# Kernel tuning notes

Hardware: AMD Instinct MI355X
Metric: run time of the kernel (lower is better)

Reference implementation:

```python
import jax, jax.numpy as jnp
import numpy as np

EPS = 1e-5
GROUPS = 8

def setup_inputs() -> dict:
    key = jax.random.key(0)
    ks = jax.random.split(key, 7)
    b, c, h, w = 32, 256, 32, 32
    x = jax.random.normal(ks[0], (b, c, h, w), dtype=jnp.float32)
    gn_w = jax.random.normal(ks[1], (c,), dtype=jnp.float32) * 0.02 + 1.0
    gn_b = jax.random.normal(ks[2], (c,), dtype=jnp.float32) * 0.02
    qkv_w = jax.random.normal(ks[3], (3 * c, c), dtype=jnp.float32) / np.sqrt(c)
    qkv_b = jax.random.normal(ks[4], (3 * c,), dtype=jnp.float32) * 0.02
    out_w = jax.random.normal(ks[5], (c, c), dtype=jnp.float32) / np.sqrt(c)
    out_b = jax.random.normal(ks[6], (c,), dtype=jnp.float32) * 0.02
    return {"x": x, "gn_w": gn_w, "gn_b": gn_b, "qkv_w": qkv_w,
            "qkv_b": qkv_b, "out_w": out_w, "out_b": out_b}

def _group_norm(x, w, b):
    B, C, H, W = x.shape
    xg = x.reshape(B, GROUPS, C // GROUPS, H, W)
    mu = jnp.mean(xg, axis=(2, 3, 4), keepdims=True)
    var = jnp.var(xg, axis=(2, 3, 4), keepdims=True)
    xn = ((xg - mu) * jax.lax.rsqrt(var + EPS)).reshape(B, C, H, W)
    return xn * w[None, :, None, None] + b[None, :, None, None]

def reference(x, gn_w, gn_b, qkv_w, qkv_b, out_w, out_b):
    b, c, h, w = x.shape
    n = h * w
    xn = _group_norm(x, gn_w, gn_b)                       # [b,c,h,w]
    # 1x1 conv == channel matmul
    qkv = jnp.einsum('bchw,oc->bohw', xn, qkv_w) + qkv_b[None, :, None, None]
    q, k, v = jnp.split(qkv, 3, axis=1)                   # each [b,c,h,w]
    q = q.reshape(b, c, n).transpose(0, 2, 1)             # [b,n,c]
    k = k.reshape(b, c, n).transpose(0, 2, 1)
    v = v.reshape(b, c, n).transpose(0, 2, 1)
    scores = jnp.einsum('bnc,bmc->bnm', q, k) / jnp.sqrt(jnp.float32(c))
    attn = jax.nn.softmax(scores, axis=-1)                # [b,n,n]
    out = jnp.einsum('bnm,bmc->bnc', attn, v)             # [b,n,c]
    out = out.transpose(0, 2, 1).reshape(b, c, h, w)
    out = jnp.einsum('bchw,oc->bohw', out, out_w) + out_b[None, :, None, None]
    # NOTE: torch code reassigns x = group_norm(x), so residual is the normalized x
    return out + xn
```

## Files before the change

kernel.cpp:

```cpp
#include <hip/hip_runtime.h>
#include <hip/hip_bf16.h>

typedef __bf16 bf16;
typedef __bf16 bf16x4 __attribute__((ext_vector_type(4)));
typedef __bf16 bf16x8 __attribute__((ext_vector_type(8)));
typedef float f32x4 __attribute__((ext_vector_type(4)));

#define B_  32
#define C_  256
#define N_  1024
#define G_  8
#define CG_ 32
#define O3_ 768

#define SWZ9(el) ((el) ^ ((((el) >> 8) & 15) << 3))
#define SWZ7(el) ((el) ^ ((((el) >> 6) & 7) << 3))

#define GLOAD16(gp, lp)                                                        \
    __builtin_amdgcn_global_load_lds(                                          \
        (const __attribute__((address_space(1))) void*)(gp),                   \
        (__attribute__((address_space(3))) void*)(lp), 16, 0, 0)

__global__ __launch_bounds__(256) void k_gnconv(const float* __restrict__ x,
                                                const float* __restrict__ w,
                                                const float* __restrict__ bia,
                                                bf16* __restrict__ xn,
                                                bf16* __restrict__ xt,
                                                const float* __restrict__ qkv_w,
                                                const float* __restrict__ out_w,
                                                bf16* __restrict__ qkv_wh,
                                                bf16* __restrict__ out_wh) {
    int blk = blockIdx.x;
    int tid = threadIdx.x;
    if (blk >= 256) {
        int i = (blk - 256) * 256 + tid;
        if (i < O3_ * C_) qkv_wh[i] = (bf16)qkv_w[i];
        if (i < C_ * C_)  out_wh[i] = (bf16)out_w[i];
        return;
    }

    extern __shared__ char smem[];
    float* xs   = (float*)smem;
    float4* xs4 = (float4*)smem;
    bf16* tile  = (bf16*)(smem + 131072);
    int b = blk >> 3, g = blk & 7;
    const float4* xb4 = (const float4*)(x + (size_t)b * C_ * N_ + (size_t)g * CG_ * N_);

    float s = 0.f, ss = 0.f;
    for (int i = tid; i < CG_ * N_ / 4; i += 256) {
        float4 v = xb4[i];
        xs4[i] = v;
        s  += v.x + v.y + v.z + v.w;
        ss += v.x * v.x + v.y * v.y + v.z * v.z + v.w * v.w;
    }
    for (int off = 32; off; off >>= 1) {
        s  += __shfl_down(s, off);
        ss += __shfl_down(ss, off);
    }
    __shared__ float red[8];
    __shared__ float stat[2];
    int wid = tid >> 6, lane = tid & 63;
    if (lane == 0) { red[wid] = s; red[wid + 4] = ss; }
    __syncthreads();
    if (tid == 0) {
        float S  = red[0] + red[1] + red[2] + red[3];
        float SS = red[4] + red[5] + red[6] + red[7];
        float mu = S / (float)(CG_ * N_);
        float var = SS / (float)(CG_ * N_) - mu * mu;
        stat[0] = mu;
        stat[1] = rsqrtf(var + 1e-5f);
    }
    __syncthreads();
    float mu = stat[0], rstd = stat[1];

    for (int nc = 0; nc < N_; nc += 256) {
        for (int i = tid; i < 2048; i += 256) {
            int cl = i >> 6, f = i & 63;
            int c = g * CG_ + cl;
            float sc = rstd * w[c], sh = bia[c] - mu * sc;
            float4 v = xs4[cl * 256 + (nc >> 2) + f];
            bf16x4 h = { (bf16)(v.x * sc + sh), (bf16)(v.y * sc + sh),
                         (bf16)(v.z * sc + sh), (bf16)(v.w * sc + sh) };
            *(bf16x4*)(xn + (size_t)b * C_ * N_ + (size_t)c * N_ + nc + f * 4) = h;
            tile[(f * 4 + 0) * 40 + cl] = h[0];
            tile[(f * 4 + 1) * 40 + cl] = h[1];
            tile[(f * 4 + 2) * 40 + cl] = h[2];
            tile[(f * 4 + 3) * 40 + cl] = h[3];
        }
        __syncthreads();
        for (int u = tid; u < 256 * 4; u += 256) {
            int nl = u >> 2, ch = u & 3;
            bf16x8 v = *(const bf16x8*)&tile[nl * 40 + ch * 8];
            *(bf16x8*)(xt + (size_t)b * N_ * C_ + (size_t)(nc + nl) * C_ + g * CG_ + ch * 8) = v;
        }
        __syncthreads();
    }
}

__global__ __launch_bounds__(256) void k_qkv(const bf16* __restrict__ xt,
                                             const bf16* __restrict__ wq,
                                             const float* __restrict__ qb,
                                             bf16* __restrict__ Qs,
                                             bf16* __restrict__ Kt,
                                             bf16* __restrict__ Vt) {
    __shared__ bf16 smem[17408];
    bf16* aT = smem;
    bf16* bT = smem + 8192;
    int nt = blockIdx.x, ot = blockIdx.y, b = blockIdx.z;
    int tid = threadIdx.x, wid = tid >> 6, lane = tid & 63;
    int wr = wid >> 1, wc = wid & 1;
    const bf16* Ab = xt + (size_t)b * N_ * C_ + (size_t)nt * 128 * C_;
    const bf16* Bb = wq + (size_t)ot * 128 * C_;

    bf16x8 areg[4], breg[4];
    #define LOAD_KT(kt)                                                        \
        for (int j = 0; j < 4; ++j) {                                          \
            int lin = (j * 256 + tid) * 8;                                     \
            int row = lin >> 6, col = lin & 63;                                \
            areg[j] = *(const bf16x8*)&Ab[(size_t)row * C_ + (kt) * 64 + col]; \
            breg[j] = *(const bf16x8*)&Bb[(size_t)row * C_ + (kt) * 64 + col]; \
        }

    f32x4 acc[4][4] = {};
    LOAD_KT(0);
    for (int kt = 0; kt < 4; ++kt) {
        for (int j = 0; j < 4; ++j) {
            int lin = (j * 256 + tid) * 8;
            *(bf16x8*)&aT[SWZ7(lin)] = areg[j];
            *(bf16x8*)&bT[SWZ7(lin)] = breg[j];
        }
        __syncthreads();
        if (kt < 3) { LOAD_KT(kt + 1); }
        for (int kk = 0; kk < 2; ++kk) {
            bf16x8 af[4], bfr[4];
            for (int m = 0; m < 4; ++m) {
                int el = (wr * 64 + m * 16 + (lane & 15)) * 64 + kk * 32 + (lane >> 4) * 8;
                af[m] = *(const bf16x8*)&aT[SWZ7(el)];
            }
            for (int n = 0; n < 4; ++n) {
                int el = (wc * 64 + n * 16 + (lane & 15)) * 64 + kk * 32 + (lane >> 4) * 8;
                bfr[n] = *(const bf16x8*)&bT[SWZ7(el)];
            }
            for (int m = 0; m < 4; ++m)
                for (int n = 0; n < 4; ++n)
                    acc[m][n] = __builtin_amdgcn_mfma_f32_16x16x32_bf16(af[m], bfr[n], acc[m][n], 0, 0, 0);
        }
        __syncthreads();
    }
    #undef LOAD_KT

    int o0 = ot * 128;
    if (ot < 4) {
        bf16* dst = (ot < 2) ? (Qs + (size_t)b * N_ * C_) : (Kt + (size_t)b * N_ * C_);
        float qsc = (ot < 2) ? 0.0625f : 1.0f;
        for (int m = 0; m < 4; ++m) for (int n = 0; n < 4; ++n) {
            int o = o0 + wc * 64 + n * 16 + (lane & 15);
            float bias = qb[o];
            int row0 = nt * 128 + wr * 64 + m * 16 + (lane >> 4) * 4;
            for (int r = 0; r < 4; ++r)
                dst[(size_t)(row0 + r) * C_ + (o & 255)] = (bf16)((acc[m][n][r] + bias) * qsc);
        }
    } else {
        bf16* tileE = smem;
        for (int m = 0; m < 4; ++m) for (int n = 0; n < 4; ++n) {
            int ol = wc * 64 + n * 16 + (lane & 15);
            float bias = qb[o0 + ol];
            int rl0 = wr * 64 + m * 16 + (lane >> 4) * 4;
            for (int r = 0; r < 4; ++r)
                tileE[(size_t)ol * 136 + rl0 + r] = (bf16)(acc[m][n][r] + bias);
        }
        __syncthreads();
        bf16* Vb = Vt + (size_t)b * C_ * N_ + (size_t)(o0 - 512) * N_ + (size_t)nt * 128;
        for (int u = tid; u < 128 * 16; u += 256) {
            int ol = u >> 4, ch = u & 15;
            bf16x8 v = *(const bf16x8*)&tileE[ol * 136 + ch * 8];
            *(bf16x8*)&Vb[(size_t)ol * N_ + ch * 8] = v;
        }
    }
}

__global__ __launch_bounds__(256, 2) void k_attn(const bf16* __restrict__ Qs,
                                                 const bf16* __restrict__ Kt,
                                                 const bf16* __restrict__ Vt,
                                                 bf16* __restrict__ Ao) {
    extern __shared__ char smem[];
    bf16*  kbuf = (bf16*)smem;
    bf16*  vbuf = (bf16*)(smem + 32768);
    bf16*  pl   = (bf16*)(smem + 65536);
    float* al   = (float*)(smem + 70656);
    int b = blockIdx.x, qb = blockIdx.y;
    int tid = threadIdx.x, wid = tid >> 6, lane = tid & 63;
    const bf16* Qb = Qs + (size_t)b * N_ * C_;
    const bf16* Kb = Kt + (size_t)b * N_ * C_;
    const bf16* Vb = Vt + (size_t)b * C_ * N_;
    int q0 = qb * 64;

    bf16x8 qf[8];
    {
        int row = q0 + wid * 16 + (lane & 15);
        const bf16* qr = Qb + (size_t)row * C_ + (lane >> 4) * 8;
        #pragma unroll
        for (int kk = 0; kk < 8; ++kk) qf[kk] = *(const bf16x8*)(qr + kk * 32);
    }

    f32x4 oac[4][4] = {};
    float lrun[4] = {0.f, 0.f, 0.f, 0.f};

    auto stage = [&](int mt, int bi) {
        int m0 = mt * 32;
        bf16* kd = kbuf + bi * 8192;
        bf16* vd = vbuf + bi * 8192;
        #pragma unroll
        for (int j = 0; j < 4; ++j) {
            int chunk = wid * 4 + j;
            int d = chunk * 512 + lane * 8;
            int ek = SWZ9(d);
            int krow = ek >> 8, kcol = ek & 255;
            GLOAD16(Kb + (size_t)(m0 + krow) * C_ + kcol, kd + chunk * 512);
            int ev = SWZ7(d);
            int kv = ev & 31;
            int ch = ((ev >> 6) << 1) | ((ev >> 5) & 1);
            GLOAD16(Vb + (size_t)ch * N_ + m0 + kv, vd + chunk * 512);
        }
    };

    stage(0, 0);
    __syncthreads();

    for (int mt = 0; mt < 32; ++mt) {
        int cur = mt & 1;
        if (mt < 31) stage(mt + 1, cur ^ 1);

        const bf16* kc = kbuf + cur * 8192;
        const bf16* vc = vbuf + cur * 8192;

        f32x4 sac[2] = {};
        __builtin_amdgcn_s_setprio(1);
        #pragma unroll
        for (int kk = 0; kk < 8; ++kk)
            #pragma unroll
            for (int n = 0; n < 2; ++n) {
                int el = (n * 16 + (lane & 15)) * 256 + kk * 32 + (lane >> 4) * 8;
                bf16x8 bfr = *(const bf16x8*)&kc[SWZ9(el)];
                sac[n] = __builtin_amdgcn_mfma_f32_16x16x32_bf16(qf[kk], bfr, sac[n], 0, 0, 0);
            }
        __builtin_amdgcn_s_setprio(0);

        #pragma unroll
        for (int r = 0; r < 4; ++r) {
            int prow = (wid * 16 + (lane >> 4) * 4 + r) * 40 + (lane & 15);
            float e0 = __expf(fminf(sac[0][r], 60.f));
            float e1 = __expf(fminf(sac[1][r], 60.f));
            lrun[r] += e0 + e1;
            pl[prow]      = (bf16)e0;
            pl[prow + 16] = (bf16)e1;
        }
        __syncthreads();

        __builtin_amdgcn_s_setprio(1);
        bf16x8 paf[4];
        #pragma unroll
        for (int m = 0; m < 4; ++m)
            paf[m] = *(const bf16x8*)&pl[(m * 16 + (lane & 15)) * 40 + (lane >> 4) * 8];
        #pragma unroll
        for (int n = 0; n < 4; ++n) {
            int ch = wid * 64 + n * 16 + (lane & 15);
            int e = (ch >> 1) * 64 + (ch & 1) * 32 + (lane >> 4) * 8;
            bf16x8 bfr = *(const bf16x8*)&vc[SWZ7(e)];
            #pragma unroll
            for (int m = 0; m < 4; ++m)
                oac[m][n] = __builtin_amdgcn_mfma_f32_16x16x32_bf16(paf[m], bfr, oac[m][n], 0, 0, 0);
        }
        __builtin_amdgcn_s_setprio(0);

        __syncthreads();
    }

    #pragma unroll
    for (int r = 0; r < 4; ++r) {
        float s = lrun[r];
        s += __shfl_xor(s, 1);
        s += __shfl_xor(s, 2);
        s += __shfl_xor(s, 4);
        s += __shfl_xor(s, 8);
        lrun[r] = s;
    }
    if (!(lane & 15)) {
        #pragma unroll
        for (int r = 0; r < 4; ++r)
            al[wid * 16 + (lane >> 4) * 4 + r] = 1.f / lrun[r];
    }
    __syncthreads();

    #pragma unroll
    for (int m = 0; m < 4; ++m)
        #pragma unroll
        for (int r = 0; r < 4; ++r) {
            float iv = al[m * 16 + (lane >> 4) * 4 + r];
            int row = q0 + m * 16 + (lane >> 4) * 4 + r;
            #pragma unroll
            for (int n = 0; n < 4; ++n)
                Ao[(size_t)b * N_ * C_ + (size_t)row * C_ + wid * 64 + n * 16 + (lane & 15)] =
                    (bf16)(oac[m][n][r] * iv);
        }
}

__global__ __launch_bounds__(256) void k_proj(const bf16* __restrict__ Ao,
                                              const bf16* __restrict__ wo,
                                              const float* __restrict__ ob,
                                              const bf16* __restrict__ xn,
                                              float* __restrict__ out) {
    __shared__ bf16 aT[128 * 64];
    __shared__ bf16 bT[128 * 64];
    int nt = blockIdx.x, ot = blockIdx.y, b = blockIdx.z;
    int tid = threadIdx.x, wid = tid >> 6, lane = tid & 63;
    int wr = wid >> 1, wc = wid & 1;
    const bf16* Abase = wo + (size_t)ot * 128 * C_;
    const bf16* Bbase = Ao + (size_t)b * N_ * C_ + (size_t)nt * 128 * C_;

    bf16x8 areg[4], breg[4];
    #define LOAD_KT(kt)                                                            \
        for (int j = 0; j < 4; ++j) {                                              \
            int lin = (j * 256 + tid) * 8;                                         \
            int row = lin >> 6, col = lin & 63;                                    \
            areg[j] = *(const bf16x8*)&Abase[(size_t)row * C_ + (kt) * 64 + col];  \
            breg[j] = *(const bf16x8*)&Bbase[(size_t)row * C_ + (kt) * 64 + col];  \
        }

    f32x4 acc[4][4] = {};
    LOAD_KT(0);
    for (int kt = 0; kt < 4; ++kt) {
        for (int j = 0; j < 4; ++j) {
            int lin = (j * 256 + tid) * 8;
            *(bf16x8*)&aT[SWZ7(lin)] = areg[j];
            *(bf16x8*)&bT[SWZ7(lin)] = breg[j];
        }
        __syncthreads();
        if (kt < 3) { LOAD_KT(kt + 1); }
        for (int kk = 0; kk < 2; ++kk) {
            bf16x8 af[4], bfr[4];
            for (int m = 0; m < 4; ++m) {
                int el = (wr * 64 + m * 16 + (lane & 15)) * 64 + kk * 32 + (lane >> 4) * 8;
                af[m] = *(const bf16x8*)&aT[SWZ7(el)];
            }
            for (int n = 0; n < 4; ++n) {
                int el = (wc * 64 + n * 16 + (lane & 15)) * 64 + kk * 32 + (lane >> 4) * 8;
                bfr[n] = *(const bf16x8*)&bT[SWZ7(el)];
            }
            for (int m = 0; m < 4; ++m)
                for (int n = 0; n < 4; ++n)
                    acc[m][n] = __builtin_amdgcn_mfma_f32_16x16x32_bf16(af[m], bfr[n], acc[m][n], 0, 0, 0);
        }
        __syncthreads();
    }
    #undef LOAD_KT

    for (int m = 0; m < 4; ++m) {
        int o0 = ot * 128 + wr * 64 + m * 16 + (lane >> 4) * 4;
        for (int n = 0; n < 4; ++n) {
            int col = nt * 128 + wc * 64 + n * 16 + (lane & 15);
            for (int r = 0; r < 4; ++r) {
                int o = o0 + r;
                float v = acc[m][n][r] + ob[o] + (float)xn[(size_t)b * C_ * N_ + (size_t)o * N_ + col];
                out[(size_t)b * C_ * N_ + (size_t)o * N_ + col] = v;
            }
        }
    }
}

extern "C" void kernel_launch(void* const* d_in, const int* in_sizes, int n_in,
                              void* d_out, int out_size, void* d_ws, size_t ws_size,
                              hipStream_t stream) {
    const float* x     = (const float*)d_in[0];
    const float* gn_w  = (const float*)d_in[1];
    const float* gn_b  = (const float*)d_in[2];
    const float* qkv_w = (const float*)d_in[3];
    const float* qkv_b = (const float*)d_in[4];
    const float* out_w = (const float*)d_in[5];
    const float* out_b = (const float*)d_in[6];
    float* out = (float*)d_out;

    char* ws = (char*)d_ws;
    size_t tensor = (size_t)B_ * C_ * N_ * 2;
    bf16* xn  = (bf16*)(ws);
    bf16* xt  = (bf16*)(ws + tensor);
    bf16* Qs  = (bf16*)(ws + 2 * tensor);
    bf16* Kt  = (bf16*)(ws + 3 * tensor);
    bf16* Vt  = (bf16*)(ws + 4 * tensor);
    bf16* Ao  = xt;
    bf16* qkv_wh = (bf16*)(ws + 5 * tensor);
    bf16* out_wh = (bf16*)(ws + 5 * tensor + (size_t)O3_ * C_ * 2);

    (void)hipFuncSetAttribute(reinterpret_cast<const void*>(&k_gnconv),
                              hipFuncAttributeMaxDynamicSharedMemorySize, 151552);
    (void)hipFuncSetAttribute(reinterpret_cast<const void*>(&k_attn),
                              hipFuncAttributeMaxDynamicSharedMemorySize, 70912);

    k_gnconv<<<1024, 256, 151552, stream>>>(x, gn_w, gn_b, xn, xt,
                                            qkv_w, out_w, qkv_wh, out_wh);
    k_qkv<<<dim3(8, 6, 32), 256, 0, stream>>>(xt, qkv_wh, qkv_b, Qs, Kt, Vt);
    k_attn<<<dim3(32, 16), 256, 70912, stream>>>(Qs, Kt, Vt, Ao);
    k_proj<<<dim3(8, 2, 32), 256, 0, stream>>>(Ao, out_wh, out_b, xn, out);
}
```

Before: 117.4 us.

## Fuse output projection and residual into attention kernel epilogue

The separate projection kernel is removed. Each attention block now writes its normalized 64x256 output tile into shared memory and multiplies it by the out-projection weights with MFMA, reading the weights straight from global memory. It then adds the bias and the normalized-input residual before storing. This saves one kernel launch and the global round-trip of the attention output. In exchange the attention kernel carries an extra GEMM epilogue with uncached weight loads and column-strided output stores.

New measurement: 112.3 us. 1.05x faster.

```diff
diff --git a/kernel.cpp b/kernel.cpp
--- a/kernel.cpp
+++ b/kernel.cpp
@@ -40,7 +40,6 @@
     }
 
     extern __shared__ char smem[];
-    float* xs   = (float*)smem;
     float4* xs4 = (float4*)smem;
     bf16* tile  = (bf16*)(smem + 131072);
     int b = blk >> 3, g = blk & 7;
@@ -182,12 +181,16 @@
 __global__ __launch_bounds__(256, 2) void k_attn(const bf16* __restrict__ Qs,
                                                  const bf16* __restrict__ Kt,
                                                  const bf16* __restrict__ Vt,
-                                                 bf16* __restrict__ Ao) {
+                                                 const bf16* __restrict__ wo,
+                                                 const float* __restrict__ ob,
+                                                 const bf16* __restrict__ xn,
+                                                 float* __restrict__ out) {
     extern __shared__ char smem[];
     bf16*  kbuf = (bf16*)smem;
     bf16*  vbuf = (bf16*)(smem + 32768);
     bf16*  pl   = (bf16*)(smem + 65536);
     float* al   = (float*)(smem + 70656);
+    bf16*  Osm  = (bf16*)smem;
     int b = blockIdx.x, qb = blockIdx.y;
     int tid = threadIdx.x, wid = tid >> 6, lane = tid & 63;
     const bf16* Qb = Qs + (size_t)b * N_ * C_;
@@ -297,72 +300,45 @@
         #pragma unroll
         for (int r = 0; r < 4; ++r) {
             float iv = al[m * 16 + (lane >> 4) * 4 + r];
-            int row = q0 + m * 16 + (lane >> 4) * 4 + r;
+            int row = m * 16 + (lane >> 4) * 4 + r;
             #pragma unroll
             for (int n = 0; n < 4; ++n)
-                Ao[(size_t)b * N_ * C_ + (size_t)row * C_ + wid * 64 + n * 16 + (lane & 15)] =
-                    (bf16)(oac[m][n][r] * iv);
-        }
-}
-
-__global__ __launch_bounds__(256) void k_proj(const bf16* __restrict__ Ao,
-                                              const bf16* __restrict__ wo,
-                                              const float* __restrict__ ob,
-                                              const bf16* __restrict__ xn,
-                                              float* __restrict__ out) {
-    __shared__ bf16 aT[128 * 64];
-    __shared__ bf16 bT[128 * 64];
-    int nt = blockIdx.x, ot = blockIdx.y, b = blockIdx.z;
-    int tid = threadIdx.x, wid = tid >> 6, lane = tid & 63;
-    int wr = wid >> 1, wc = wid & 1;
-    const bf16* Abase = wo + (size_t)ot * 128 * C_;
-    const bf16* Bbase = Ao + (size_t)b * N_ * C_ + (size_t)nt * 128 * C_;
-
-    bf16x8 areg[4], breg[4];
-    #define LOAD_KT(kt)                                                            \
-        for (int j = 0; j < 4; ++j) {                                              \
-            int lin = (j * 256 + tid) * 8;                                         \
-            int row = lin >> 6, col = lin & 63;                                    \
-            areg[j] = *(const bf16x8*)&Abase[(size_t)row * C_ + (kt) * 64 + col];  \
-            breg[j] = *(const bf16x8*)&Bbase[(size_t)row * C_ + (kt) * 64 + col];  \
-        }
-
-    f32x4 acc[4][4] = {};
-    LOAD_KT(0);
-    for (int kt = 0; kt < 4; ++kt) {
-        for (int j = 0; j < 4; ++j) {
-            int lin = (j * 256 + tid) * 8;
-            *(bf16x8*)&aT[SWZ7(lin)] = areg[j];
-            *(bf16x8*)&bT[SWZ7(lin)] = breg[j];
-        }
-        __syncthreads();
-        if (kt < 3) { LOAD_KT(kt + 1); }
-        for (int kk = 0; kk < 2; ++kk) {
+                Osm[row * 260 + wid * 64 + n * 16 + (lane & 15)] = (bf16)(oac[m][n][r] * iv);
+        }
+    __syncthreads();
+
+    {
+        f32x4 acc[4][4] = {};
+        const bf16* wob = wo + (size_t)wid * 64 * C_;
+        #pragma unroll
+        for (int kk = 0; kk < 8; ++kk) {
             bf16x8 af[4], bfr[4];
-            for (int m = 0; m < 4; ++m) {
-                int el = (wr * 64 + m * 16 + (lane & 15)) * 64 + kk * 32 + (lane >> 4) * 8;
-                af[m] = *(const bf16x8*)&aT[SWZ7(el)];
-            }
-            for (int n = 0; n < 4; ++n) {
-                int el = (wc * 64 + n * 16 + (lane & 15)) * 64 + kk * 32 + (lane >> 4) * 8;
-                bfr[n] = *(const bf16x8*)&bT[SWZ7(el)];
-            }
+            #pragma unroll
             for (int m = 0; m < 4; ++m)
+                af[m] = *(const bf16x8*)&wob[(size_t)(m * 16 + (lane & 15)) * C_ + kk * 32 + (lane >> 4) * 8];
+            #pragma unroll
+            for (int n = 0; n < 4; ++n)
+                bfr[n] = *(const bf16x8*)&Osm[(n * 16 + (lane & 15)) * 260 + kk * 32 + (lane >> 4) * 8];
+            #pragma unroll
+            for (int m = 0; m < 4; ++m)
+                #pragma unroll
                 for (int n = 0; n < 4; ++n)
                     acc[m][n] = __builtin_amdgcn_mfma_f32_16x16x32_bf16(af[m], bfr[n], acc[m][n], 0, 0, 0);
         }
-        __syncthreads();
-    }
-    #undef LOAD_KT
-
-    for (int m = 0; m < 4; ++m) {
-        int o0 = ot * 128 + wr * 64 + m * 16 + (lane >> 4) * 4;
-        for (int n = 0; n < 4; ++n) {
-            int col = nt * 128 + wc * 64 + n * 16 + (lane & 15);
+        #pragma unroll
+        for (int m = 0; m < 4; ++m) {
+            int o0 = wid * 64 + m * 16 + (lane >> 4) * 4;
+            #pragma unroll
             for (int r = 0; r < 4; ++r) {
                 int o = o0 + r;
-                float v = acc[m][n][r] + ob[o] + (float)xn[(size_t)b * C_ * N_ + (size_t)o * N_ + col];
-                out[(size_t)b * C_ * N_ + (size_t)o * N_ + col] = v;
+                float bias = ob[o];
+                const bf16* xr = xn + (size_t)b * C_ * N_ + (size_t)o * N_ + q0;
+                float* orow = out + (size_t)b * C_ * N_ + (size_t)o * N_ + q0;
+                #pragma unroll
+                for (int n = 0; n < 4; ++n) {
+                    int col = n * 16 + (lane & 15);
+                    orow[col] = acc[m][n][r] + bias + (float)xr[col];
+                }
             }
         }
     }
@@ -387,7 +363,6 @@
     bf16* Qs  = (bf16*)(ws + 2 * tensor);
     bf16* Kt  = (bf16*)(ws + 3 * tensor);
     bf16* Vt  = (bf16*)(ws + 4 * tensor);
-    bf16* Ao  = xt;
     bf16* qkv_wh = (bf16*)(ws + 5 * tensor);
     bf16* out_wh = (bf16*)(ws + 5 * tensor + (size_t)O3_ * C_ * 2);
 
@@ -399,6 +374,5 @@
     k_gnconv<<<1024, 256, 151552, stream>>>(x, gn_w, gn_b, xn, xt,
                                             qkv_w, out_w, qkv_wh, out_wh);
     k_qkv<<<dim3(8, 6, 32), 256, 0, stream>>>(xt, qkv_wh, qkv_b, Qs, Kt, Vt);
-    k_attn<<<dim3(32, 16), 256, 70912, stream>>>(Qs, Kt, Vt, Ao);
-    k_proj<<<dim3(8, 2, 32), 256, 0, stream>>>(Ao, out_wh, out_b, xn, out);
+    k_attn<<<dim3(32, 16), 256, 70912, stream>>>(Qs, Kt, Vt, out_wh, out_b, xn, out);
 }
```
